# Performance work log

Hardware: AMD Instinct MI355X
Metric: run time of the kernel (lower is better)

Reference implementation:

```python
import jax, jax.numpy as jnp
import numpy as np

N_BITS_W = 8      # weight quant bits
N_BITS_A = 8      # activation quant bits
SCALE_RANGE_IN = 1.0
BN_EPS = 1e-5
ACT_THRES = 6.0   # ReLUN clamp


def _fake_quant(v, n_bits, scaling_range):
    """Symmetric uniform fake-quantization with straight-through estimator.
    Layer-wise scale from the max-abs value (Qmodes.layer_wise)."""
    qp = float(2 ** (n_bits - 1) - 1)
    alpha = scaling_range * jnp.max(jnp.abs(v))
    step = alpha / qp
    q = jnp.clip(jnp.round(v / step), -qp, qp) * step
    # STE: forward uses q, gradient flows through v unchanged
    return v + jax.lax.stop_gradient(q - v)


def setup_inputs() -> dict:
    key = jax.random.key(0)
    k1, k2 = jax.random.split(key)
    x = jax.random.normal(k1, (32, 16, 224, 224), dtype=jnp.float32)
    # Kaiming-ish scale for a 3x3 conv with 16 in-channels
    weight = jax.random.normal(k2, (16, 16, 3, 3), dtype=jnp.float32) * (1.0 / np.sqrt(16 * 9))
    gamma = jnp.ones((16,), dtype=jnp.float32)
    beta = jnp.zeros((16,), dtype=jnp.float32)
    return {"x": x, "weight": weight, "gamma": gamma, "beta": beta}


def reference(x, weight, gamma, beta):
    # --- GemmConv2d with quant_flag=True, noise_flag=False ---
    xq = _fake_quant(x, N_BITS_A, SCALE_RANGE_IN)
    wq = _fake_quant(weight, N_BITS_W, 1.0)
    y = jax.lax.conv_general_dilated(
        xq, wq,
        window_strides=(1, 1),
        padding=[(1, 1), (1, 1)],
        dimension_numbers=("NCHW", "OIHW", "NCHW"),
    )  # [N, Cout, H, W]
    # --- BatchNorm2d (training mode: batch statistics, biased variance) ---
    mean = jnp.mean(y, axis=(0, 2, 3))
    var = jnp.var(y, axis=(0, 2, 3))
    inv = gamma * jax.lax.rsqrt(var + BN_EPS)
    y = y * inv[None, :, None, None] + (beta - mean * inv)[None, :, None, None]
    # --- ReLUN(6): clamp to [0, act_thres] ---
    return jnp.clip(y, 0.0, ACT_THRES)
```

## Files before the change

### kernel.cpp

```cpp
#include <hip/hip_runtime.h>
#include <stdint.h>

#define QP 127.0f
#define HW2 50176
#define NPIX 1605632
#define NELEM 25690112
#define ABS_GRID 2048
#define NRG 56
#define NBLK_CONV 1792

#define WS_WQ    256
#define WS_BMAX  4096
#define WS_PART  16384
#define WS_XQ    (1 << 20)

typedef int v4i __attribute__((ext_vector_type(4)));

__device__ __forceinline__ void stage_strip(const int4* __restrict__ xq,
                                            int4* sXs, int n, int r0, int tid) {
  #pragma unroll
  for (int j = 0; j < 6; ++j) {
    int g = r0 - 1 + j;
    if (tid < 224) {
      int4 v = {0, 0, 0, 0};
      if ((unsigned)g < 224u) v = xq[(n * 224 + g) * 224 + tid];
      sXs[j * 226 + 1 + tid] = v;
    } else if (tid < 226) {
      int4 z = {0, 0, 0, 0};
      sXs[j * 226 + ((tid == 224) ? 0 : 225)] = z;
    }
  }
}

__device__ __forceinline__ void conv_lane_setup(const int4* __restrict__ wq4,
                                                int ccol, int chunk,
                                                v4i (&bfrag)[3], int (&abase)[3]) {
  #pragma unroll
  for (int m = 0; m < 3; ++m) {
    int tap = 4 * m + chunk;
    v4i bv = {0, 0, 0, 0};
    if (tap <= 8) {
      int4 t = wq4[ccol * 9 + tap];
      bv[0] = t.x; bv[1] = t.y; bv[2] = t.z; bv[3] = t.w;
    }
    bfrag[m] = bv;
    int tc = (tap > 8) ? 8 : tap;
    int kh = tc / 3, kw = tc - kh * 3;
    abase[m] = kh * 226 + ccol + kw;
  }
}

__global__ __launch_bounds__(256) void k_absmax_wq(const float* __restrict__ x,
                                                   const float* __restrict__ w,
                                                   char* __restrict__ ws) {
  __shared__ float red[4];
  __shared__ float s_sw;
  float* hdr_f = (float*)ws;
  float* bmax = (float*)(ws + WS_BMAX);
  int* wq = (int*)(ws + WS_WQ);
  const int tid = threadIdx.x;

  const float4* x4 = (const float4*)x;
  float m = 0.0f;
  for (int i = blockIdx.x * 256 + tid; i < NELEM / 4; i += ABS_GRID * 256) {
    float4 v = x4[i];
    m = fmaxf(m, fmaxf(fmaxf(fabsf(v.x), fabsf(v.y)),
                       fmaxf(fabsf(v.z), fabsf(v.w))));
  }
  #pragma unroll
  for (int off = 32; off; off >>= 1) m = fmaxf(m, __shfl_down(m, off, 64));
  if ((tid & 63) == 0) red[tid >> 6] = m;
  __syncthreads();
  if (tid == 0)
    bmax[blockIdx.x] = fmaxf(fmaxf(red[0], red[1]), fmaxf(red[2], red[3]));

  if (blockIdx.x == 0) {
    __syncthreads();
    float mw = 0.0f;
    for (int i = tid; i < 2304; i += 256) mw = fmaxf(mw, fabsf(w[i]));
    #pragma unroll
    for (int off = 32; off; off >>= 1) mw = fmaxf(mw, __shfl_down(mw, off, 64));
    if ((tid & 63) == 0) red[tid >> 6] = mw;
    __syncthreads();
    if (tid == 0) {
      float sw = fmaxf(fmaxf(red[0], red[1]), fmaxf(red[2], red[3])) / QP;
      hdr_f[1] = sw;
      s_sw = sw;
    }
    __syncthreads();
    float sw = s_sw;
    for (int i = tid; i < 576; i += 256) {
      int cout = i / 36; int r = i - cout * 36;
      int tap = r >> 2;  int c4 = r & 3;
      int kh = tap / 3, kw = tap - kh * 3;
      unsigned bits = 0;
      #pragma unroll
      for (int j = 0; j < 4; ++j) {
        int cin = c4 * 4 + j;
        float v = w[((cout * 16 + cin) * 3 + kh) * 3 + kw];
        int q = (int)rintf(v / sw);
        q = max(-127, min(127, q));
        bits |= ((unsigned)(q & 0xff)) << (8 * j);
      }
      wq[i] = (int)bits;
    }
  }
}

__global__ __launch_bounds__(256) void k_quant_x(const float* __restrict__ x,
                                                 char* __restrict__ ws) {
  __shared__ float sRed4[4];
  const float* __restrict__ bmax = (const float*)(ws + WS_BMAX);
  float* hdr_f = (float*)ws;
  int4* xq = (int4*)(ws + WS_XQ);
  const int tid = threadIdx.x;

  float m = 0.0f;
  for (int i = tid; i < ABS_GRID; i += 256) m = fmaxf(m, bmax[i]);
  #pragma unroll
  for (int off = 32; off; off >>= 1) m = fmaxf(m, __shfl_down(m, off, 64));
  if ((tid & 63) == 0) sRed4[tid >> 6] = m;
  __syncthreads();
  const float sx =
      fmaxf(fmaxf(sRed4[0], sRed4[1]), fmaxf(sRed4[2], sRed4[3])) / QP;
  if (blockIdx.x == 0 && tid == 0) hdr_f[2] = sx;

  int t = blockIdx.x * 256 + tid;
  int p0 = t * 4;
  int n = p0 / HW2;
  int hw = p0 - n * HW2;
  const float4* xb = (const float4*)(x + (size_t)n * 16 * HW2 + hw);
  unsigned comp[4][4];
  #pragma unroll
  for (int j = 0; j < 4; ++j)
    #pragma unroll
    for (int k = 0; k < 4; ++k) comp[j][k] = 0u;
  #pragma unroll
  for (int c = 0; c < 16; ++c) {
    float4 vc = xb[c * (HW2 / 4)];
    float f[4] = {vc.x, vc.y, vc.z, vc.w};
    #pragma unroll
    for (int j = 0; j < 4; ++j) {
      int q = (int)rintf(f[j] / sx);
      q = max(-127, min(127, q));
      comp[j][c >> 2] |= ((unsigned)(q & 0xff)) << (8 * (c & 3));
    }
  }
  #pragma unroll
  for (int j = 0; j < 4; ++j) {
    int4 v;
    v.x = (int)comp[j][0]; v.y = (int)comp[j][1];
    v.z = (int)comp[j][2]; v.w = (int)comp[j][3];
    xq[p0 + j] = v;
  }
}

__global__ __launch_bounds__(256) void k_conv_stats(const char* __restrict__ ws,
                                                    float* __restrict__ partials) {
  __shared__ int4 sXs[6 * 226];
  __shared__ int   sS[4][16];
  __shared__ float sQ[4][16];
  const int4* __restrict__ xq = (const int4*)(ws + WS_XQ);
  const int4* __restrict__ wq4 = (const int4*)(ws + WS_WQ);

  const int tid = threadIdx.x;
  const int b = blockIdx.x;
  const int n = b / NRG, rg = b - n * NRG;
  const int r0 = rg * 4;

  stage_strip(xq, sXs, n, r0, tid);

  const int lane = tid & 63, wid = tid >> 6;
  const int ccol = lane & 15, chunk = lane >> 4;
  v4i bfrag[3];
  int abase[3];
  conv_lane_setup(wq4, ccol, chunk, bfrag, abase);
  __syncthreads();

  int   sAcc = 0;
  float qAcc = 0.0f;
  for (int t = wid; t < 56; t += 4) {
    int ty = t / 14, x0 = (t - ty * 14) << 4;
    int off = ty * 226 + x0;
    v4i acc = {0, 0, 0, 0};
    #pragma unroll
    for (int m = 0; m < 3; ++m) {
      int4 av = sXs[off + abase[m]];
      v4i a; a[0] = av.x; a[1] = av.y; a[2] = av.z; a[3] = av.w;
      acc = __builtin_amdgcn_mfma_i32_16x16x64_i8(a, bfrag[m], acc, 0, 0, 0);
    }
    #pragma unroll
    for (int r = 0; r < 4; ++r) {
      int d = acc[r];
      sAcc += d;
      float f = (float)d;
      qAcc += f * f;
    }
  }
  sAcc += __shfl_xor(sAcc, 16, 64);
  sAcc += __shfl_xor(sAcc, 32, 64);
  qAcc += __shfl_xor(qAcc, 16, 64);
  qAcc += __shfl_xor(qAcc, 32, 64);
  if (lane < 16) { sS[wid][ccol] = sAcc; sQ[wid][ccol] = qAcc; }
  __syncthreads();
  if (tid < 32) {
    int c = tid & 15;
    float t;
    if (tid < 16) t = (float)(sS[0][c] + sS[1][c] + sS[2][c] + sS[3][c]);
    else          t = sQ[0][c] + sQ[1][c] + sQ[2][c] + sQ[3][c];
    partials[b * 32 + tid] = t;
  }
}

__global__ void k_finalize(const float* __restrict__ partials,
                           const float* __restrict__ gamma,
                           const float* __restrict__ beta,
                           float* __restrict__ hdr_f) {
  __shared__ double sdd[256][4];
  __shared__ double sfin[32];
  int t = threadIdx.x;
  const float4* p4 = (const float4*)partials;
  double d0 = 0, d1 = 0, d2 = 0, d3 = 0;
  #pragma unroll 8
  for (int k = 0; k < 56; ++k) {
    float4 v = p4[t + 256 * k];
    d0 += (double)v.x; d1 += (double)v.y; d2 += (double)v.z; d3 += (double)v.w;
  }
  sdd[t][0] = d0; sdd[t][1] = d1; sdd[t][2] = d2; sdd[t][3] = d3;
  __syncthreads();
  if (t < 32) {
    double s = 0.0;
    #pragma unroll 8
    for (int i = 0; i < 32; ++i) s += sdd[(t >> 2) + 8 * i][t & 3];
    sfin[t] = s;
  }
  __syncthreads();
  if (t < 16) {
    float sf = hdr_f[2] * hdr_f[1];
    double s = (double)sf;
    const double M = (double)NPIX;
    double mean = s * sfin[t] / M;
    double ey2 = s * s * sfin[16 + t] / M;
    double var = ey2 - mean * mean;
    double inv = (double)gamma[t] / sqrt(var + 1e-5);
    hdr_f[16 + t] = (float)(s * inv);
    hdr_f[32 + t] = (float)((double)beta[t] - mean * inv);
  }
}

__global__ __launch_bounds__(256) void k_conv_out(const char* __restrict__ ws,
                                                  float* __restrict__ out) {
  __shared__ int4 sXs[6 * 226];
  const int4* __restrict__ xq = (const int4*)(ws + WS_XQ);
  const int4* __restrict__ wq4 = (const int4*)(ws + WS_WQ);
  const float* hdr_f = (const float*)ws;

  const int tid = threadIdx.x;
  const int b = blockIdx.x;
  const int n = b / NRG, rg = b - n * NRG;
  const int r0 = rg * 4;

  stage_strip(xq, sXs, n, r0, tid);

  const int lane = tid & 63, wid = tid >> 6;
  const int ccol = lane & 15, chunk = lane >> 4;
  v4i bfrag[3];
  int abase[3];
  conv_lane_setup(wq4, ccol, chunk, bfrag, abase);
  const float Af = hdr_f[16 + ccol];
  const float Bf = hdr_f[32 + ccol];
  __syncthreads();

  float* oplane = out + ((size_t)n * 16 + ccol) * HW2;
  for (int t = wid; t < 56; t += 4) {
    int ty = t / 14, x0 = (t - ty * 14) << 4;
    int off = ty * 226 + x0;
    v4i acc = {0, 0, 0, 0};
    #pragma unroll
    for (int m = 0; m < 3; ++m) {
      int4 av = sXs[off + abase[m]];
      v4i a; a[0] = av.x; a[1] = av.y; a[2] = av.z; a[3] = av.w;
      acc = __builtin_amdgcn_mfma_i32_16x16x64_i8(a, bfrag[m], acc, 0, 0, 0);
    }
    float4 o;
    float v0 = fminf(fmaxf(fmaf((float)acc[0], Af, Bf), 0.0f), 6.0f);
    float v1 = fminf(fmaxf(fmaf((float)acc[1], Af, Bf), 0.0f), 6.0f);
    float v2 = fminf(fmaxf(fmaf((float)acc[2], Af, Bf), 0.0f), 6.0f);
    float v3 = fminf(fmaxf(fmaf((float)acc[3], Af, Bf), 0.0f), 6.0f);
    o.x = v0; o.y = v1; o.z = v2; o.w = v3;
    int y = r0 + ty, xb = x0 + chunk * 4;
    *(float4*)&oplane[y * 224 + xb] = o;
  }
}

extern "C" void kernel_launch(void* const* d_in, const int* in_sizes, int n_in,
                              void* d_out, int out_size, void* d_ws, size_t ws_size,
                              hipStream_t stream) {
  const float* x = (const float*)d_in[0];
  const float* w = (const float*)d_in[1];
  const float* gamma = (const float*)d_in[2];
  const float* beta = (const float*)d_in[3];
  float* out = (float*)d_out;
  char* ws = (char*)d_ws;
  float* partials = (float*)(ws + WS_PART);

  k_absmax_wq<<<ABS_GRID, 256, 0, stream>>>(x, w, ws);
  k_quant_x<<<1568, 256, 0, stream>>>(x, ws);
  k_conv_stats<<<NBLK_CONV, 256, 0, stream>>>(ws, partials);
  k_finalize<<<1, 256, 0, stream>>>(partials, gamma, beta, (float*)ws);
  k_conv_out<<<NBLK_CONV, 256, 0, stream>>>(ws, out);
}
```

Baseline: 239.5 us.

## Fuse activation quantization into conv-stats kernel and replace finalize with atomics

```diff
diff --git a/kernel.cpp b/kernel.cpp
--- a/kernel.cpp
+++ b/kernel.cpp
@@ -10,8 +10,9 @@
 #define NBLK_CONV 1792
 
 #define WS_WQ    256
+#define WS_SSUM  2560
+#define WS_QSUM  2688
 #define WS_BMAX  4096
-#define WS_PART  16384
 #define WS_XQ    (1 << 20)
 
 typedef int v4i __attribute__((ext_vector_type(4)));
@@ -59,6 +60,11 @@
   float* bmax = (float*)(ws + WS_BMAX);
   int* wq = (int*)(ws + WS_WQ);
   const int tid = threadIdx.x;
+
+  if (blockIdx.x == 0 && tid < 16) {
+    ((unsigned long long*)(ws + WS_SSUM))[tid] = 0ull;
+    ((double*)(ws + WS_QSUM))[tid] = 0.0;
+  }
 
   const float4* x4 = (const float4*)x;
   float m = 0.0f;
@@ -107,10 +113,14 @@
   }
 }
 
-__global__ __launch_bounds__(256) void k_quant_x(const float* __restrict__ x,
-                                                 char* __restrict__ ws) {
+__global__ __launch_bounds__(256) void k_quant_stats(const float* __restrict__ x,
+                                                     char* __restrict__ ws) {
+  __shared__ int4 sXs[6 * 226];
+  __shared__ int   sS[4][16];
+  __shared__ float sQ[4][16];
   __shared__ float sRed4[4];
   const float* __restrict__ bmax = (const float*)(ws + WS_BMAX);
+  const int4* __restrict__ wq4 = (const int4*)(ws + WS_WQ);
   float* hdr_f = (float*)ws;
   int4* xq = (int4*)(ws + WS_XQ);
   const int tid = threadIdx.x;
@@ -125,50 +135,52 @@
       fmaxf(fmaxf(sRed4[0], sRed4[1]), fmaxf(sRed4[2], sRed4[3])) / QP;
   if (blockIdx.x == 0 && tid == 0) hdr_f[2] = sx;
 
-  int t = blockIdx.x * 256 + tid;
-  int p0 = t * 4;
-  int n = p0 / HW2;
-  int hw = p0 - n * HW2;
-  const float4* xb = (const float4*)(x + (size_t)n * 16 * HW2 + hw);
-  unsigned comp[4][4];
-  #pragma unroll
-  for (int j = 0; j < 4; ++j)
-    #pragma unroll
-    for (int k = 0; k < 4; ++k) comp[j][k] = 0u;
-  #pragma unroll
-  for (int c = 0; c < 16; ++c) {
-    float4 vc = xb[c * (HW2 / 4)];
-    float f[4] = {vc.x, vc.y, vc.z, vc.w};
-    #pragma unroll
-    for (int j = 0; j < 4; ++j) {
-      int q = (int)rintf(f[j] / sx);
-      q = max(-127, min(127, q));
-      comp[j][c >> 2] |= ((unsigned)(q & 0xff)) << (8 * (c & 3));
-    }
-  }
-  #pragma unroll
-  for (int j = 0; j < 4; ++j) {
-    int4 v;
-    v.x = (int)comp[j][0]; v.y = (int)comp[j][1];
-    v.z = (int)comp[j][2]; v.w = (int)comp[j][3];
-    xq[p0 + j] = v;
-  }
-}
-
-__global__ __launch_bounds__(256) void k_conv_stats(const char* __restrict__ ws,
-                                                    float* __restrict__ partials) {
-  __shared__ int4 sXs[6 * 226];
-  __shared__ int   sS[4][16];
-  __shared__ float sQ[4][16];
-  const int4* __restrict__ xq = (const int4*)(ws + WS_XQ);
-  const int4* __restrict__ wq4 = (const int4*)(ws + WS_WQ);
-
-  const int tid = threadIdx.x;
   const int b = blockIdx.x;
   const int n = b / NRG, rg = b - n * NRG;
   const int r0 = rg * 4;
 
-  stage_strip(xq, sXs, n, r0, tid);
+  for (int task = tid; task < 336; task += 256) {
+    int j = task / 56, g = task - j * 56;
+    int gr = r0 - 1 + j;
+    int4 v[4] = {{0,0,0,0}, {0,0,0,0}, {0,0,0,0}, {0,0,0,0}};
+    if ((unsigned)gr < 224u) {
+      const float4* xb = (const float4*)x + (size_t)n * 16 * (HW2 / 4)
+                         + gr * 56 + g;
+      unsigned comp[4][4];
+      #pragma unroll
+      for (int k = 0; k < 4; ++k)
+        #pragma unroll
+        for (int q4 = 0; q4 < 4; ++q4) comp[k][q4] = 0u;
+      #pragma unroll
+      for (int c = 0; c < 16; ++c) {
+        float4 vc = xb[c * (HW2 / 4)];
+        float f[4] = {vc.x, vc.y, vc.z, vc.w};
+        #pragma unroll
+        for (int k = 0; k < 4; ++k) {
+          int q = (int)rintf(f[k] / sx);
+          q = max(-127, min(127, q));
+          comp[k][c >> 2] |= ((unsigned)(q & 0xff)) << (8 * (c & 3));
+        }
+      }
+      #pragma unroll
+      for (int k = 0; k < 4; ++k) {
+        v[k].x = (int)comp[k][0]; v[k].y = (int)comp[k][1];
+        v[k].z = (int)comp[k][2]; v[k].w = (int)comp[k][3];
+      }
+      if (j >= 1 && j <= 4) {
+        #pragma unroll
+        for (int k = 0; k < 4; ++k)
+          xq[(n * 224 + gr) * 224 + 4 * g + k] = v[k];
+      }
+    }
+    #pragma unroll
+    for (int k = 0; k < 4; ++k) sXs[j * 226 + 1 + 4 * g + k] = v[k];
+  }
+  if (tid >= 244) {
+    int idx = tid - 244;
+    int4 z = {0, 0, 0, 0};
+    sXs[(idx >> 1) * 226 + ((idx & 1) ? 225 : 0)] = z;
+  }
 
   const int lane = tid & 63, wid = tid >> 6;
   const int ccol = lane & 15, chunk = lane >> 4;
@@ -184,10 +196,10 @@
     int off = ty * 226 + x0;
     v4i acc = {0, 0, 0, 0};
     #pragma unroll
-    for (int m = 0; m < 3; ++m) {
-      int4 av = sXs[off + abase[m]];
+    for (int m3 = 0; m3 < 3; ++m3) {
+      int4 av = sXs[off + abase[m3]];
       v4i a; a[0] = av.x; a[1] = av.y; a[2] = av.z; a[3] = av.w;
-      acc = __builtin_amdgcn_mfma_i32_16x16x64_i8(a, bfrag[m], acc, 0, 0, 0);
+      acc = __builtin_amdgcn_mfma_i32_16x16x64_i8(a, bfrag[m3], acc, 0, 0, 0);
     }
     #pragma unroll
     for (int r = 0; r < 4; ++r) {
@@ -203,54 +215,24 @@
   qAcc += __shfl_xor(qAcc, 32, 64);
   if (lane < 16) { sS[wid][ccol] = sAcc; sQ[wid][ccol] = qAcc; }
   __syncthreads();
-  if (tid < 32) {
+  if (tid < 16) {
+    int c = tid;
+    long long s4 = (long long)sS[0][c] + sS[1][c] + sS[2][c] + sS[3][c];
+    atomicAdd(((unsigned long long*)(ws + WS_SSUM)) + c,
+              (unsigned long long)s4);
+  } else if (tid < 32) {
     int c = tid & 15;
-    float t;
-    if (tid < 16) t = (float)(sS[0][c] + sS[1][c] + sS[2][c] + sS[3][c]);
-    else          t = sQ[0][c] + sQ[1][c] + sQ[2][c] + sQ[3][c];
-    partials[b * 32 + tid] = t;
-  }
-}
-
-__global__ void k_finalize(const float* __restrict__ partials,
-                           const float* __restrict__ gamma,
-                           const float* __restrict__ beta,
-                           float* __restrict__ hdr_f) {
-  __shared__ double sdd[256][4];
-  __shared__ double sfin[32];
-  int t = threadIdx.x;
-  const float4* p4 = (const float4*)partials;
-  double d0 = 0, d1 = 0, d2 = 0, d3 = 0;
-  #pragma unroll 8
-  for (int k = 0; k < 56; ++k) {
-    float4 v = p4[t + 256 * k];
-    d0 += (double)v.x; d1 += (double)v.y; d2 += (double)v.z; d3 += (double)v.w;
-  }
-  sdd[t][0] = d0; sdd[t][1] = d1; sdd[t][2] = d2; sdd[t][3] = d3;
-  __syncthreads();
-  if (t < 32) {
-    double s = 0.0;
-    #pragma unroll 8
-    for (int i = 0; i < 32; ++i) s += sdd[(t >> 2) + 8 * i][t & 3];
-    sfin[t] = s;
-  }
-  __syncthreads();
-  if (t < 16) {
-    float sf = hdr_f[2] * hdr_f[1];
-    double s = (double)sf;
-    const double M = (double)NPIX;
-    double mean = s * sfin[t] / M;
-    double ey2 = s * s * sfin[16 + t] / M;
-    double var = ey2 - mean * mean;
-    double inv = (double)gamma[t] / sqrt(var + 1e-5);
-    hdr_f[16 + t] = (float)(s * inv);
-    hdr_f[32 + t] = (float)((double)beta[t] - mean * inv);
+    float q4 = sQ[0][c] + sQ[1][c] + sQ[2][c] + sQ[3][c];
+    atomicAdd(((double*)(ws + WS_QSUM)) + c, (double)q4);
   }
 }
 
 __global__ __launch_bounds__(256) void k_conv_out(const char* __restrict__ ws,
+                                                  const float* __restrict__ gamma,
+                                                  const float* __restrict__ beta,
                                                   float* __restrict__ out) {
   __shared__ int4 sXs[6 * 226];
+  __shared__ float sAB[32];
   const int4* __restrict__ xq = (const int4*)(ws + WS_XQ);
   const int4* __restrict__ wq4 = (const int4*)(ws + WS_WQ);
   const float* hdr_f = (const float*)ws;
@@ -261,15 +243,31 @@
   const int r0 = rg * 4;
 
   stage_strip(xq, sXs, n, r0, tid);
+
+  if (tid < 16) {
+    unsigned long long us = ((const unsigned long long*)(ws + WS_SSUM))[tid];
+    double S = (double)(long long)us;
+    double Q = ((const double*)(ws + WS_QSUM))[tid];
+    float sf = hdr_f[2] * hdr_f[1];
+    double s = (double)sf;
+    const double M = (double)NPIX;
+    double mean = s * S / M;
+    double ey2 = s * s * Q / M;
+    double var = ey2 - mean * mean;
+    double inv = (double)gamma[tid] / sqrt(var + 1e-5);
+    sAB[tid] = (float)(s * inv);
+    sAB[16 + tid] = (float)((double)beta[tid] - mean * inv);
+  }
 
   const int lane = tid & 63, wid = tid >> 6;
   const int ccol = lane & 15, chunk = lane >> 4;
   v4i bfrag[3];
   int abase[3];
   conv_lane_setup(wq4, ccol, chunk, bfrag, abase);
-  const float Af = hdr_f[16 + ccol];
-  const float Bf = hdr_f[32 + ccol];
-  __syncthreads();
+  __syncthreads();
+
+  const float Af = sAB[ccol];
+  const float Bf = sAB[16 + ccol];
 
   float* oplane = out + ((size_t)n * 16 + ccol) * HW2;
   for (int t = wid; t < 56; t += 4) {
@@ -277,17 +275,16 @@
     int off = ty * 226 + x0;
     v4i acc = {0, 0, 0, 0};
     #pragma unroll
-    for (int m = 0; m < 3; ++m) {
-      int4 av = sXs[off + abase[m]];
+    for (int m3 = 0; m3 < 3; ++m3) {
+      int4 av = sXs[off + abase[m3]];
       v4i a; a[0] = av.x; a[1] = av.y; a[2] = av.z; a[3] = av.w;
-      acc = __builtin_amdgcn_mfma_i32_16x16x64_i8(a, bfrag[m], acc, 0, 0, 0);
+      acc = __builtin_amdgcn_mfma_i32_16x16x64_i8(a, bfrag[m3], acc, 0, 0, 0);
     }
     float4 o;
-    float v0 = fminf(fmaxf(fmaf((float)acc[0], Af, Bf), 0.0f), 6.0f);
-    float v1 = fminf(fmaxf(fmaf((float)acc[1], Af, Bf), 0.0f), 6.0f);
-    float v2 = fminf(fmaxf(fmaf((float)acc[2], Af, Bf), 0.0f), 6.0f);
-    float v3 = fminf(fmaxf(fmaf((float)acc[3], Af, Bf), 0.0f), 6.0f);
-    o.x = v0; o.y = v1; o.z = v2; o.w = v3;
+    o.x = fminf(fmaxf(fmaf((float)acc[0], Af, Bf), 0.0f), 6.0f);
+    o.y = fminf(fmaxf(fmaf((float)acc[1], Af, Bf), 0.0f), 6.0f);
+    o.z = fminf(fmaxf(fmaf((float)acc[2], Af, Bf), 0.0f), 6.0f);
+    o.w = fminf(fmaxf(fmaf((float)acc[3], Af, Bf), 0.0f), 6.0f);
     int y = r0 + ty, xb = x0 + chunk * 4;
     *(float4*)&oplane[y * 224 + xb] = o;
   }
@@ -302,11 +299,8 @@
   const float* beta = (const float*)d_in[3];
   float* out = (float*)d_out;
   char* ws = (char*)d_ws;
-  float* partials = (float*)(ws + WS_PART);
 
   k_absmax_wq<<<ABS_GRID, 256, 0, stream>>>(x, w, ws);
-  k_quant_x<<<1568, 256, 0, stream>>>(x, ws);
-  k_conv_stats<<<NBLK_CONV, 256, 0, stream>>>(ws, partials);
-  k_finalize<<<1, 256, 0, stream>>>(partials, gamma, beta, (float*)ws);
-  k_conv_out<<<NBLK_CONV, 256, 0, stream>>>(ws, out);
-}
+  k_quant_stats<<<NBLK_CONV, 256, 0, stream>>>(x, ws);
+  k_conv_out<<<NBLK_CONV, 256, 0, stream>>>(ws, gamma, beta, out);
+}
```

Result: slower. 276.0 us (+15.2%).
